# Performance work log

Measured on AMD Instinct MI355X. Metric: run time of the kernel, lower is better.

The kernel has to match this reference:

```python
import jax, jax.numpy as jnp
import numpy as np

B, N, STEPS = 256, 2048, 64
DT = 0.1  # integration step size


def setup_inputs() -> dict:
    key = jax.random.key(0)
    ks = jax.random.split(key, 7)
    lim = 1.0 / np.sqrt(N)            # torch Linear default init bound
    kstd = np.sqrt(2.0) * np.sqrt(2.0 / N)  # custom kaiming_init std (gain*sqrt(2/size))
    return {
        "x0": jax.random.normal(ks[0], (B, N), dtype=jnp.float32),
        "free_inds": jnp.ones((B, N), dtype=jnp.float32),
        "W_w": jax.random.uniform(ks[1], (N, N), jnp.float32, -lim, lim),
        "W_b": jax.random.uniform(ks[2], (N,), jnp.float32, -lim, lim),
        "T_w": jax.random.uniform(ks[3], (N, N), jnp.float32, -lim, lim),
        "T_b": jax.random.uniform(ks[4], (N,), jnp.float32, -lim, lim),
        "w_proc_to_syn": jax.random.normal(ks[5], (N,), jnp.float32) * kstd,
        "w_syn_to_proc": jax.random.normal(ks[6], (N,), jnp.float32) * kstd,
    }


def reference(x0, free_inds, W_w, W_b, T_w, T_b, w_proc_to_syn, w_syn_to_proc):
    # Faithful to the torch forward: s0/p0 are ignored, x = s = p = x0.
    def step(carry, _):
        x, s, p = carry
        phi = jax.nn.relu(x)   # processing activation
        g = jax.nn.relu(s)     # synaptic gate
        psi = jax.nn.relu(p)   # plasticity activation
        dx = -x + (g * phi) @ W_w.T + W_b
        ds = -s + w_proc_to_syn * psi + phi
        dp = -p + psi @ T_w.T + T_b + w_syn_to_proc * g
        x_n = x + DT * dx * free_inds
        s_n = p + DT * ds   # note: s update uses p as the base, as in the source
        p_n = p + DT * dp
        return (x_n, s_n, p_n), x_n

    (x, s, p), xs = jax.lax.scan(step, (x0, x0, x0), None, length=STEPS)
    return x, xs  # xs: [STEPS, B, N]
```

## Files before the change

kernel.cpp:

```cpp
#include <hip/hip_runtime.h>
#include <hip/hip_bf16.h>

#define BB 256
#define NN 2048
#define NSTEPS 64
#define DT_C 0.1f
#define WSCALE 512.0f
#define ASCALE 8.0f
#define ACC_INV (1.0f / 4096.0f)

#define SLOT (1u << 20)
#define PSOFF (1u << 19)

typedef __attribute__((ext_vector_type(4))) float floatx4;
typedef __attribute__((ext_vector_type(4))) float f32x4;

__device__ __forceinline__ floatx4 mfma_fp8(long long a, long long b, floatx4 c) {
  return __builtin_amdgcn_mfma_f32_16x16x32_fp8_fp8(a, b, c, 0, 0, 0);
}

__device__ __forceinline__ unsigned pack4_fp8(float a, float b, float c, float d) {
  int lo = __builtin_amdgcn_cvt_pk_fp8_f32(a, b, 0, false);
  int r  = __builtin_amdgcn_cvt_pk_fp8_f32(c, d, lo, true);
  return (unsigned)r;
}
__device__ __forceinline__ unsigned char fp8byte(float v) {
  return (unsigned char)(__builtin_amdgcn_cvt_pk_fp8_f32(v, 0.f, 0, false) & 0xff);
}

__device__ __forceinline__ long long sysload(const long long* p) {
  return __hip_atomic_load(p, __ATOMIC_RELAXED, __HIP_MEMORY_SCOPE_SYSTEM);
}
__device__ __forceinline__ void sysstore(unsigned* p, unsigned v) {
  __hip_atomic_store(p, v, __ATOMIC_RELAXED, __HIP_MEMORY_SCOPE_SYSTEM);
}
template <bool C>
__device__ __forceinline__ long long aload(const long long* p) {
  if constexpr (C) return *p;
  else return sysload(p);
}


__global__ __launch_bounds__(256) void convert_kernel(
    const float* __restrict__ Ww, unsigned char* __restrict__ Wf,
    const float* __restrict__ Tw, unsigned char* __restrict__ Tf, int half) {
  int bid = blockIdx.x;
  const float* src = Ww;
  unsigned char* dst = Wf;
  if (bid >= half) { bid -= half; src = Tw; dst = Tf; }
  const int g = bid * 256 + threadIdx.x;
  const int frag = g >> 6, l = g & 63;
  const int j = (frag >> 6) * 16 + (l & 15);
  const int k = (frag & 63) * 32 + (l >> 4) * 8;
  const float* s = src + (size_t)j * NN + k;
  unsigned lo = pack4_fp8(s[0] * WSCALE, s[1] * WSCALE, s[2] * WSCALE, s[3] * WSCALE);
  unsigned hi = pack4_fp8(s[4] * WSCALE, s[5] * WSCALE, s[6] * WSCALE, s[7] * WSCALE);
  ((unsigned long long*)dst)[g] = ((unsigned long long)hi << 32) | lo;
}

__global__ __launch_bounds__(256) void init_kernel(
    const float* __restrict__ x0, unsigned char* __restrict__ Ab) {
  const int i = blockIdx.x * 256 + threadIdx.x;
  const int b = i >> 11, j = i & (NN - 1);
  const float r = fmaxf(x0[i], 0.f);
  const int dl = (b & 15) | (((j >> 3) & 3) << 4);
  const size_t fo = ((size_t)((b >> 4) * 64 + (j >> 5))) * 512 + dl * 8 + (j & 7);
  Ab[fo] = fp8byte(ASCALE * r * r);
  Ab[PSOFF + fo] = fp8byte(ASCALE * r);
}

#define LOADST(S, kc) \
  S##a0 = aload<CACHED>(aP0 + (size_t)(kc) * 64); \
  S##a1 = aload<CACHED>(aP1 + (size_t)(kc) * 64); \
  S##b0 = bP0[(size_t)(kc) * 64]; \
  S##b1 = bP1[(size_t)(kc) * 64]; \
  S##b2 = bP2[(size_t)(kc) * 64]; \
  S##b3 = bP3[(size_t)(kc) * 64];
#define DOMFMA(S) \
  acc00 = mfma_fp8(S##a0, S##b0, acc00); acc01 = mfma_fp8(S##a0, S##b1, acc01); \
  acc02 = mfma_fp8(S##a0, S##b2, acc02); acc03 = mfma_fp8(S##a0, S##b3, acc03); \
  acc10 = mfma_fp8(S##a1, S##b0, acc10); acc11 = mfma_fp8(S##a1, S##b1, acc11); \
  acc12 = mfma_fp8(S##a1, S##b2, acc12); acc13 = mfma_fp8(S##a1, S##b3, acc13);

template <bool CACHED>
__global__ __launch_bounds__(512) void fused_kernel(
    const unsigned char* __restrict__ Wf, const unsigned char* __restrict__ Tf,
    const float* __restrict__ Wb, const float* __restrict__ Tb,
    const float* __restrict__ wp2s, const float* __restrict__ ws2p,
    const float* __restrict__ fri, const float* __restrict__ x0,
    unsigned char* __restrict__ Ab,
    float* __restrict__ out, unsigned* __restrict__ bar) {
  __shared__ float eb[8][32][68];

  if constexpr (CACHED)
    __builtin_amdgcn_fence(__ATOMIC_ACQUIRE, "agent");

  const int tid = threadIdx.x;
  const int lane = tid & 63, wv = tid >> 6;
  const int lane15 = lane & 15, kq = lane >> 4;
  const int g = wv >> 2, h = wv & 3;

  const int x = blockIdx.x & 7, ii = blockIdx.x >> 3;
  const int colt = x * 4 + (ii & 3), rowt = ii >> 2;
  const int b0 = rowt * 32, j0 = colt * 64;

  const int erow = tid >> 4;
  const int c4 = (tid & 15) << 2;
  const int ej = j0 + c4;
  const size_t eidx = (size_t)(b0 + erow) * NN + ej;
  const f32x4 Wb4 = *(const f32x4*)(Wb + ej);
  const f32x4 Tb4 = *(const f32x4*)(Tb + ej);
  const f32x4 wp4 = *(const f32x4*)(wp2s + ej);
  const f32x4 ws4 = *(const f32x4*)(ws2p + ej);
  const f32x4 fr4 = *(const f32x4*)(fri + eidx);
  f32x4 xcur = *(const f32x4*)(x0 + eidx);
  f32x4 scur = xcur, pcur = xcur;

  const int bb = b0 + erow;
  const int dl = (bb & 15) | (((ej >> 3) & 3) << 4);
  const size_t fob = ((size_t)((bb >> 4) * 64 + (ej >> 5))) * 512 + dl * 8 + (ej & 7);

  const int rf0 = rowt * 2;
  const int cf0 = colt * 4;
  const int kcb = h * 16;
  const unsigned char* Bfm = g == 0 ? Wf : Tf;
  const long long* bP0 = (const long long*)Bfm + ((size_t)(cf0 + 0) * 64 + kcb) * 64 + lane;
  const long long* bP1 = (const long long*)Bfm + ((size_t)(cf0 + 1) * 64 + kcb) * 64 + lane;
  const long long* bP2 = (const long long*)Bfm + ((size_t)(cf0 + 2) * 64 + kcb) * 64 + lane;
  const long long* bP3 = (const long long*)Bfm + ((size_t)(cf0 + 3) * 64 + kcb) * 64 + lane;
  const size_t aOff0 = ((size_t)(rf0 + 0) * 64 + kcb) * 64 + lane;
  const size_t aOff1 = ((size_t)(rf0 + 1) * 64 + kcb) * 64 + lane;

  float* xs = out + (size_t)BB * NN;

  for (int t = 0; t < NSTEPS; ++t) {
    const unsigned rs  = CACHED ? (unsigned)t : (unsigned)(t & 1);
    const unsigned wsl = CACHED ? (unsigned)(t + 1) : (unsigned)((t + 1) & 1);
    const unsigned char* Abase = Ab + (size_t)rs * SLOT;
    const unsigned char* Ar = Abase + (g == 0 ? 0u : PSOFF);
    unsigned char* Uw  = Ab + (size_t)wsl * SLOT;
    unsigned char* PSw = Uw + PSOFF;
    const long long* aP0 = (const long long*)Ar + aOff0;
    const long long* aP1 = (const long long*)Ar + aOff1;

    floatx4 acc00 = {0.f,0.f,0.f,0.f}, acc01 = {0.f,0.f,0.f,0.f};
    floatx4 acc02 = {0.f,0.f,0.f,0.f}, acc03 = {0.f,0.f,0.f,0.f};
    floatx4 acc10 = {0.f,0.f,0.f,0.f}, acc11 = {0.f,0.f,0.f,0.f};
    floatx4 acc12 = {0.f,0.f,0.f,0.f}, acc13 = {0.f,0.f,0.f,0.f};

    long long Aa0, Aa1, Ab0, Ab1, Ab2, Ab3;
    long long Ba0, Ba1, Bb0, Bb1, Bb2, Bb3;
    long long Ca0, Ca1, Cb0, Cb1, Cb2, Cb3;
    long long Da0, Da1, Db0, Db1, Db2, Db3;
    LOADST(A, 0) LOADST(B, 1) LOADST(C, 2) LOADST(D, 3)
    for (int kc = 0; kc < 12; kc += 4) {
      DOMFMA(A) LOADST(A, kc + 4)
      DOMFMA(B) LOADST(B, kc + 5)
      DOMFMA(C) LOADST(C, kc + 6)
      DOMFMA(D) LOADST(D, kc + 7)
    }
    DOMFMA(A) DOMFMA(B) DOMFMA(C) DOMFMA(D)

#pragma unroll
    for (int r = 0; r < 4; ++r) {
      eb[wv][kq * 4 + r][lane15]      = acc00[r];
      eb[wv][kq * 4 + r][16 + lane15] = acc01[r];
      eb[wv][kq * 4 + r][32 + lane15] = acc02[r];
      eb[wv][kq * 4 + r][48 + lane15] = acc03[r];
      eb[wv][16 + kq * 4 + r][lane15]      = acc10[r];
      eb[wv][16 + kq * 4 + r][16 + lane15] = acc11[r];
      eb[wv][16 + kq * 4 + r][32 + lane15] = acc12[r];
      eb[wv][16 + kq * 4 + r][48 + lane15] = acc13[r];
    }
    __syncthreads();

    f32x4 m1, m2;
    {
      const f32x4 p0 = *(const f32x4*)&eb[0][erow][c4];
      const f32x4 p1 = *(const f32x4*)&eb[1][erow][c4];
      const f32x4 p2 = *(const f32x4*)&eb[2][erow][c4];
      const f32x4 p3 = *(const f32x4*)&eb[3][erow][c4];
      const f32x4 q0 = *(const f32x4*)&eb[4][erow][c4];
      const f32x4 q1 = *(const f32x4*)&eb[5][erow][c4];
      const f32x4 q2 = *(const f32x4*)&eb[6][erow][c4];
      const f32x4 q3 = *(const f32x4*)&eb[7][erow][c4];
      m1 = ((p0 + p1) + (p2 + p3)) * ACC_INV;
      m2 = ((q0 + q1) + (q2 + q3)) * ACC_INV;
    }
    float uf[4], pf[4];
#pragma unroll
    for (int e = 0; e < 4; ++e) {
      const float xv = xcur[e], s = scur[e], p = pcur[e];
      const float phi = fmaxf(xv, 0.f), gg = fmaxf(s, 0.f), psi = fmaxf(p, 0.f);
      const float xn = xv + DT_C * (-xv + m1[e] + Wb4[e]) * fr4[e];
      const float sn = p + DT_C * (-s + wp4[e] * psi + phi);
      const float pn = p + DT_C * (-p + m2[e] + Tb4[e] + ws4[e] * gg);
      xcur[e] = xn; scur[e] = sn; pcur[e] = pn;
      uf[e] = ASCALE * fmaxf(xn, 0.f) * fmaxf(sn, 0.f);
      pf[e] = ASCALE * fmaxf(pn, 0.f);
    }
    __builtin_nontemporal_store(xcur, (f32x4*)(xs + (size_t)t * BB * NN + eidx));
    if (t == NSTEPS - 1) {
      __builtin_nontemporal_store(xcur, (f32x4*)(out + eidx));
    } else {
      sysstore((unsigned*)(Uw + fob), pack4_fp8(uf[0], uf[1], uf[2], uf[3]));
      sysstore((unsigned*)(PSw + fob), pack4_fp8(pf[0], pf[1], pf[2], pf[3]));
      asm volatile("s_waitcnt vmcnt(0)" ::: "memory");
      __syncthreads();
      if (tid == 0) {
        unsigned* leaf = bar + 32 * (1 + x);
        const unsigned v = __hip_atomic_fetch_add(leaf, 1u, __ATOMIC_RELAXED,
                                                  __HIP_MEMORY_SCOPE_AGENT);
        if (v + 1 == 32u * (unsigned)(t + 1))
          __hip_atomic_fetch_add(bar, 1u, __ATOMIC_RELAXED, __HIP_MEMORY_SCOPE_AGENT);
        while (__hip_atomic_load(bar, __ATOMIC_RELAXED, __HIP_MEMORY_SCOPE_AGENT)
               < 8u * (unsigned)(t + 1))
          __builtin_amdgcn_s_sleep(1);
      }
      __syncthreads();
    }
  }
}

extern "C" void kernel_launch(void* const* d_in, const int* in_sizes, int n_in,
                              void* d_out, int out_size, void* d_ws, size_t ws_size,
                              hipStream_t stream) {
  const float* x0   = (const float*)d_in[0];
  const float* fri  = (const float*)d_in[1];
  const float* Ww   = (const float*)d_in[2];
  const float* Wb   = (const float*)d_in[3];
  const float* Tw   = (const float*)d_in[4];
  const float* Tb   = (const float*)d_in[5];
  const float* wp2s = (const float*)d_in[6];
  const float* ws2p = (const float*)d_in[7];
  float* out = (float*)d_out;

  const size_t BN = (size_t)BB * NN;
  const size_t NW = (size_t)NN * NN;

  const size_t needCached = 4096 + 64 * (size_t)SLOT + 2 * NW;
  const bool cached = ws_size >= needCached;
  const size_t nslots = cached ? 64 : 2;

  unsigned* bar = (unsigned*)d_ws;
  unsigned char* Abuf = (unsigned char*)d_ws + 4096;
  unsigned char* Wf = Abuf + nslots * (size_t)SLOT;
  unsigned char* Tf = Wf + NW;

  hipMemsetAsync(bar, 0, 4096, stream);
  const int chalf = (int)(NW / 2048);
  convert_kernel<<<2 * chalf, 256, 0, stream>>>(Ww, Wf, Tw, Tf, chalf);
  init_kernel<<<(int)(BN / 256), 256, 0, stream>>>(x0, Abuf);

  void* kargs[] = {
    (void*)&Wf, (void*)&Tf, (void*)&Wb, (void*)&Tb, (void*)&wp2s, (void*)&ws2p,
    (void*)&fri, (void*)&x0, (void*)&Abuf, (void*)&out, (void*)&bar
  };
  if (cached) {
    hipLaunchCooperativeKernel((const void*)fused_kernel<true>, dim3(256),
                               dim3(512), kargs, 0, stream);
  } else {
    hipLaunchCooperativeKernel((const void*)fused_kernel<false>, dim3(256),
                               dim3(512), kargs, 0, stream);
  }
}
```

Baseline: 550.9 us.

## Replace global barrier with per-row-tile flag sync and defer xs store

In the cached path, each block now publishes a per-step flag, and waits only on the 32 flags of its own row tile instead of on a full-grid hierarchical barrier. This relies on each row tile depending only on activations written by blocks in the same row tile. The xs trajectory store is moved after the flag publish so it overlaps the wait. The non-cached path keeps the tree barrier, with its counters shifted past the new flag area; this depends on the barrier buffer being large and zeroed correctly.

```diff
diff --git a/kernel.cpp b/kernel.cpp
--- a/kernel.cpp
+++ b/kernel.cpp
@@ -29,6 +29,9 @@
 }
 
 __device__ __forceinline__ long long sysload(const long long* p) {
+  return __hip_atomic_load(p, __ATOMIC_RELAXED, __HIP_MEMORY_SCOPE_SYSTEM);
+}
+__device__ __forceinline__ unsigned sysloadu(const unsigned* p) {
   return __hip_atomic_load(p, __ATOMIC_RELAXED, __HIP_MEMORY_SCOPE_SYSTEM);
 }
 __device__ __forceinline__ void sysstore(unsigned* p, unsigned v) {
@@ -136,8 +139,7 @@
   for (int t = 0; t < NSTEPS; ++t) {
     const unsigned rs  = CACHED ? (unsigned)t : (unsigned)(t & 1);
     const unsigned wsl = CACHED ? (unsigned)(t + 1) : (unsigned)((t + 1) & 1);
-    const unsigned char* Abase = Ab + (size_t)rs * SLOT;
-    const unsigned char* Ar = Abase + (g == 0 ? 0u : PSOFF);
+    const unsigned char* Ar = Ab + (size_t)rs * SLOT + (g == 0 ? 0u : PSOFF);
     unsigned char* Uw  = Ab + (size_t)wsl * SLOT;
     unsigned char* PSw = Uw + PSOFF;
     const long long* aP0 = (const long long*)Ar + aOff0;
@@ -199,25 +201,41 @@
       uf[e] = ASCALE * fmaxf(xn, 0.f) * fmaxf(sn, 0.f);
       pf[e] = ASCALE * fmaxf(pn, 0.f);
     }
-    __builtin_nontemporal_store(xcur, (f32x4*)(xs + (size_t)t * BB * NN + eidx));
     if (t == NSTEPS - 1) {
+      __builtin_nontemporal_store(xcur, (f32x4*)(xs + (size_t)t * BB * NN + eidx));
       __builtin_nontemporal_store(xcur, (f32x4*)(out + eidx));
     } else {
       sysstore((unsigned*)(Uw + fob), pack4_fp8(uf[0], uf[1], uf[2], uf[3]));
       sysstore((unsigned*)(PSw + fob), pack4_fp8(pf[0], pf[1], pf[2], pf[3]));
       asm volatile("s_waitcnt vmcnt(0)" ::: "memory");
       __syncthreads();
-      if (tid == 0) {
-        unsigned* leaf = bar + 32 * (1 + x);
-        const unsigned v = __hip_atomic_fetch_add(leaf, 1u, __ATOMIC_RELAXED,
-                                                  __HIP_MEMORY_SCOPE_AGENT);
-        if (v + 1 == 32u * (unsigned)(t + 1))
-          __hip_atomic_fetch_add(bar, 1u, __ATOMIC_RELAXED, __HIP_MEMORY_SCOPE_AGENT);
-        while (__hip_atomic_load(bar, __ATOMIC_RELAXED, __HIP_MEMORY_SCOPE_AGENT)
-               < 8u * (unsigned)(t + 1))
-          __builtin_amdgcn_s_sleep(1);
+      if constexpr (CACHED) {
+        if (tid == 0)
+          sysstore(bar + rowt * 32 + colt, (unsigned)(t + 1));
+        __builtin_nontemporal_store(xcur,
+            (f32x4*)(xs + (size_t)t * BB * NN + eidx));
+        if (wv == 0) {
+          const unsigned* fp = bar + rowt * 32 + (lane & 31);
+          while (sysloadu(fp) < (unsigned)(t + 1))
+            __builtin_amdgcn_s_sleep(1);
+        }
+        __syncthreads();
+      } else {
+        __builtin_nontemporal_store(xcur,
+            (f32x4*)(xs + (size_t)t * BB * NN + eidx));
+        if (tid == 0) {
+          unsigned* leaf = bar + 512 + 32 * (1 + x);
+          const unsigned v = __hip_atomic_fetch_add(leaf, 1u, __ATOMIC_RELAXED,
+                                                    __HIP_MEMORY_SCOPE_AGENT);
+          if (v + 1 == 32u * (unsigned)(t + 1))
+            __hip_atomic_fetch_add(bar + 512, 1u, __ATOMIC_RELAXED,
+                                   __HIP_MEMORY_SCOPE_AGENT);
+          while (__hip_atomic_load(bar + 512, __ATOMIC_RELAXED,
+                                   __HIP_MEMORY_SCOPE_AGENT) < 8u * (unsigned)(t + 1))
+            __builtin_amdgcn_s_sleep(1);
+        }
+        __syncthreads();
       }
-      __syncthreads();
     }
   }
 }
```

New measurement: 598.2 us. 8.6% more time.
